# Kernel optimization log

Hardware: AMD Instinct MI355X
Metric: run time of the kernel (lower is better)

The kernel has to match this reference:

```python
import jax, jax.numpy as jnp
import numpy as np

EPS = 1e-5

def setup_inputs() -> dict:
    key = jax.random.key(0)
    k1, k2, k3 = jax.random.split(key, 3)
    B, T, D, K = 8, 4096, 256, 2048
    x = jax.random.normal(k1, (B, T, D), dtype=jnp.float32)
    embedding_sum = jax.random.normal(k2, (K, D), dtype=jnp.float32)
    cluster_usage = jax.random.uniform(k3, (K,), dtype=jnp.float32)
    return {"x": x, "embedding_sum": embedding_sum, "cluster_usage": cluster_usage}

def reference(x, embedding_sum, cluster_usage):
    # embedding = embedding_sum / clamp(cluster_usage, eps)  -> [K, D]
    emb = embedding_sum / jnp.clip(cluster_usage, EPS, None)[:, None]
    shape = x.shape
    flat = x.reshape(-1, shape[-1])  # [N, D]
    # squared Euclidean distances (argmin-equivalent to torch.cdist p=2)
    d = (
        jnp.sum(flat * flat, axis=-1, keepdims=True)
        - 2.0 * flat @ emb.T
        + jnp.sum(emb * emb, axis=-1)
    )  # [N, K]
    flat_codes = jnp.argmin(d, axis=-1)  # [N]
    codes = flat_codes.reshape(shape[:-1])  # [B, T]
    quantized = emb[codes]  # [B, T, D]
    return quantized, codes
```

## Files before the change

kernel.cpp:

```cpp
#include <hip/hip_runtime.h>


#define EPSV 1e-5f
#define TAU  0.4f
#define DDIM 256
#define BM   128
#define BCL  128
#define NPART 4
#define NCT  4
#define RPB  8
#define KSPL 4
#define NROWS 32768
#define EB   32

typedef __attribute__((ext_vector_type(8))) _Float16 f16x8;
typedef __attribute__((ext_vector_type(4))) float f32x4;
typedef unsigned short u16;
typedef unsigned u32;
typedef unsigned long long u64;

__device__ __forceinline__ u16 f2h(float f) {
    f = fminf(fmaxf(f, -60000.f), 60000.f);
    const _Float16 h = (_Float16)f;
    return __builtin_bit_cast(u16, h);
}
__device__ __forceinline__ u32 umn(u32 a, u32 b) { return a < b ? a : b; }
__device__ __forceinline__ u32 umx(u32 a, u32 b) { return a > b ? a : b; }
__device__ __forceinline__ float unsort(u32 u) {
    const u32 v = (u & 0x80000000u) ? (u & 0x7FFFFFFFu) : ~u;
    return __builtin_bit_cast(float, v);
}
__device__ __forceinline__ u64 packdk(float d, int k) {
    u32 u = __builtin_bit_cast(u32, d);
    u = (u & 0x80000000u) ? ~u : (u | 0x80000000u);
    return ((u64)u << 32) | (u32)k;
}

__global__ void prep(const float* __restrict__ esum,
                     const float* __restrict__ usage,
                     const float* __restrict__ x,
                     float* __restrict__ emb_t,
                     u16* __restrict__ eh,
                     float* __restrict__ enorm2,
                     u16* __restrict__ xh,
                     int* __restrict__ counter,
                     int K) {
    const int b = blockIdx.x;
    const int NEB = K / EB;
    if (b == 0 && threadIdx.x == 0) *counter = 0;
    if (b < NEB) {
        __shared__ float tile[EB][DDIM + 1];
        const int k0 = b * EB;
        const int d  = threadIdx.x;
        for (int r = 0; r < EB; ++r) {
            const int k = k0 + r;
            const float u = fmaxf(usage[k], EPSV);
            const float e = esum[(size_t)k * DDIM + d] / u;
            tile[r][d] = e;
            eh[(size_t)k * DDIM + d] = f2h(e);
        }
        __syncthreads();
        if (threadIdx.x < EB) {
            const int r = threadIdx.x;
            float s = 0.f;
            #pragma unroll 8
            for (int dd = 0; dd < DDIM; ++dd) {
                const float e = tile[r][dd];
                s = fmaf(e, e, s);
            }
            enorm2[k0 + r] = s;
        }
        for (int it = 0; it < DDIM / 8; ++it) {
            const int dd   = it * 8 + (threadIdx.x >> 5);
            const int lane = threadIdx.x & 31;
            emb_t[(size_t)dd * K + k0 + lane] = tile[lane][dd];
        }
    } else {
        const int n = (b - NEB) * 4 + (threadIdx.x >> 6);
        const int l = threadIdx.x & 63;
        const float4 v = *(const float4*)&x[(size_t)n * DDIM + l * 4];
        ushort4 h;
        h.x = f2h(v.x); h.y = f2h(v.y); h.z = f2h(v.z); h.w = f2h(v.w);
        *(ushort4*)&xh[(size_t)n * DDIM + l * 4] = h;
    }
}

__global__ __launch_bounds__(256, 2) void vq_mfma(
        const u16* __restrict__ xh, const u16* __restrict__ eh,
        const float* __restrict__ enorm2,
        u32* __restrict__ pp1, u32* __restrict__ pp2, int N) {
    __shared__ __align__(16) u16 Als[BM * 64];
    __shared__ __align__(16) u16 Bls[BCL * 64];

    const int tid = threadIdx.x;
    const int l   = tid & 63;
    const int w   = tid >> 6;
    const int wr  = w >> 1, wc = w & 1;

    const int nwg = (N / BM) * NPART;
    const int q   = nwg >> 3;
    const int pb  = blockIdx.x;
    const int logical = (pb & 7) * q + (pb >> 3);
    const int rowblk  = logical >> 2;
    const int part    = logical & 3;
    const int n0      = rowblk * BM;
    const int cbase   = part * 512;

    u32 m1p[4][4], m2p[4][4];
    #pragma unroll
    for (int a = 0; a < 4; ++a)
        #pragma unroll
        for (int b = 0; b < 4; ++b) { m1p[a][b] = 0xFFFFFFFFu; m2p[a][b] = 0xFFFFFFFFu; }

    const int sgc = (l & 7) ^ ((l >> 3) & 7);

    for (int ct = 0; ct < NCT; ++ct) {
        const int c0 = cbase + ct * BCL;
        f32x4 acc[4][4];
        #pragma unroll
        for (int a = 0; a < 4; ++a)
            #pragma unroll
            for (int b = 0; b < 4; ++b) acc[a][b] = (f32x4){0.f, 0.f, 0.f, 0.f};

        for (int ch = 0; ch < 4; ++ch) {
            const int colof = ch * 64;

            __syncthreads();
            #pragma unroll
            for (int j = 0; j < 4; ++j) {
                const int r = (w * 4 + j) * 8 + (l >> 3);
                const u16* ga = xh + (size_t)(n0 + r) * DDIM + colof + sgc * 8;
                __builtin_amdgcn_global_load_lds(
                    (const __attribute__((address_space(1))) void*)ga,
                    (__attribute__((address_space(3))) void*)((char*)Als + (w * 4 + j) * 1024),
                    16, 0, 0);
            }
            #pragma unroll
            for (int j = 0; j < 4; ++j) {
                const int r = (w * 4 + j) * 8 + (l >> 3);
                const u16* gb = eh + (size_t)(c0 + r) * DDIM + colof + sgc * 8;
                __builtin_amdgcn_global_load_lds(
                    (const __attribute__((address_space(1))) void*)gb,
                    (__attribute__((address_space(3))) void*)((char*)Bls + (w * 4 + j) * 1024),
                    16, 0, 0);
            }
            __syncthreads();

            #pragma unroll
            for (int ks = 0; ks < 2; ++ks) {
                f16x8 af[4], bfr[4];
                #pragma unroll
                for (int f = 0; f < 4; ++f) {
                    const int arow = wr * 64 + f * 16 + (l & 15);
                    const int ac   = (ks * 4 + (l >> 4)) ^ (l & 7);
                    af[f] = *(const f16x8*)((const char*)Als + arow * 128 + ac * 16);
                    const int brow = wc * 64 + f * 16 + (l & 15);
                    const int bc   = (ks * 4 + (l >> 4)) ^ (l & 7);
                    bfr[f] = *(const f16x8*)((const char*)Bls + brow * 128 + bc * 16);
                }
                #pragma unroll
                for (int fm = 0; fm < 4; ++fm)
                    #pragma unroll
                    for (int fn = 0; fn < 4; ++fn)
                        acc[fm][fn] = __builtin_amdgcn_mfma_f32_16x16x32_f16(
                            af[fm], bfr[fn], acc[fm][fn], 0, 0, 0);
            }
        }

        #pragma unroll
        for (int fn = 0; fn < 4; ++fn) {
            const int k = c0 + wc * 64 + fn * 16 + (l & 15);
            const float en = enorm2[k];
            #pragma unroll
            for (int fm = 0; fm < 4; ++fm)
                #pragma unroll
                for (int i = 0; i < 4; ++i) {
                    const float s = fmaf(-2.0f, acc[fm][fn][i], en);
                    u32 u = __builtin_bit_cast(u32, s);
                    u = ((int)u < 0) ? ~u : (u | 0x80000000u);
                    const u32 p = (u & 0xFFFFF800u) | (u32)k;
                    m2p[fm][i] = umn(m2p[fm][i], umx(p, m1p[fm][i]));
                    m1p[fm][i] = umn(m1p[fm][i], p);
                }
        }
    }

    #pragma unroll
    for (int fm = 0; fm < 4; ++fm)
        #pragma unroll
        for (int i = 0; i < 4; ++i) {
            u32 p1 = m1p[fm][i], p2 = m2p[fm][i];
            #pragma unroll
            for (int mask = 1; mask < 16; mask <<= 1) {
                const u32 o1 = (u32)__shfl_xor((int)p1, mask, 64);
                const u32 o2 = (u32)__shfl_xor((int)p2, mask, 64);
                p2 = umn(umn(p2, o2), umx(p1, o1));
                p1 = umn(p1, o1);
            }
            m1p[fm][i] = p1; m2p[fm][i] = p2;
        }

    __syncthreads();
    u32* S1 = (u32*)Als;
    u32* S2 = (u32*)((char*)Als + 512);
    if (wc == 0 && (l & 15) == 0) {
        #pragma unroll
        for (int fm = 0; fm < 4; ++fm)
            #pragma unroll
            for (int i = 0; i < 4; ++i) {
                const int r = wr * 64 + fm * 16 + (l >> 4) * 4 + i;
                S1[r] = m1p[fm][i]; S2[r] = m2p[fm][i];
            }
    }
    __syncthreads();
    if (wc == 1 && (l & 15) == 0) {
        #pragma unroll
        for (int fm = 0; fm < 4; ++fm)
            #pragma unroll
            for (int i = 0; i < 4; ++i) {
                const int r = wr * 64 + fm * 16 + (l >> 4) * 4 + i;
                const u32 o1 = S1[r], o2 = S2[r];
                u32 p1 = m1p[fm][i], p2 = m2p[fm][i];
                const u32 M2 = umn(umn(p2, o2), umx(p1, o1));
                const u32 M1 = umn(p1, o1);
                const int n = n0 + r;
                pp1[(size_t)part * N + n] = M1;
                pp2[(size_t)part * N + n] = M2;
            }
    }
}

__global__ void combine(const u32* __restrict__ pp1, const u32* __restrict__ pp2,
                        int* __restrict__ codes_i, int* __restrict__ flags,
                        int* __restrict__ list, int* __restrict__ counter,
                        u64* __restrict__ packed, int N) {
    const int n = blockIdx.x * 256 + threadIdx.x;
    u32 p1 = pp1[n], p2 = pp2[n];
    #pragma unroll
    for (int j = 1; j < NPART; ++j) {
        const u32 o1 = pp1[(size_t)j * N + n], o2 = pp2[(size_t)j * N + n];
        p2 = umn(umn(p2, o2), umx(p1, o1));
        p1 = umn(p1, o1);
    }
    codes_i[n] = (int)(p1 & 0x7FFu);
    const float m1f = unsort(p1 & 0xFFFFF800u);
    const float m2f = unsort(p2 & 0xFFFFF800u);
    const int fl = (m2f - m1f < TAU) ? 1 : 0;
    flags[n] = fl;
    if (fl) {
        packed[n] = 0xFFFFFFFFFFFFFFFFull;
        const int idx = atomicAdd(counter, 1);
        list[idx] = n;
    }
}

__global__ __launch_bounds__(256) void rescue_c(
        const float* __restrict__ x, const float* __restrict__ emb_t,
        const float* __restrict__ enorm2,
        const int* __restrict__ list, const int* __restrict__ counter,
        u64* __restrict__ packed, int K) {
    __shared__ float xs[RPB][DDIM];
    const int t = threadIdx.x;
    const int l = t & 63;
    int cnt = *counter;
    cnt = cnt < 0 ? 0 : (cnt > NROWS ? NROWS : cnt);
    if (cnt == 0) return;
    const int nblk  = (cnt + RPB - 1) / RPB;
    const int items = nblk * KSPL;
    const int kc    = K / KSPL;

    for (int wi = blockIdx.x; wi < items; wi += gridDim.x) {
        const int g = wi >> 2;
        const int q = wi & 3;
        const int base = g * RPB;
        int rows[RPB];
        #pragma unroll
        for (int r = 0; r < RPB; ++r) {
            int idx = base + r;
            rows[r] = list[idx < cnt ? idx : cnt - 1];
        }
        __syncthreads();
        #pragma unroll
        for (int r = 0; r < RPB; ++r)
            xs[r][t] = x[(size_t)rows[r] * DDIM + t];
        __syncthreads();

        float acc[RPB][2];
        #pragma unroll
        for (int r = 0; r < RPB; ++r) { acc[r][0] = 0.f; acc[r][1] = 0.f; }

        const float* eb = emb_t + q * kc + 2 * t;
        #pragma unroll 4
        for (int d = 0; d < DDIM; ++d) {
            const float2 e = *(const float2*)&eb[(size_t)d * K];
            #pragma unroll
            for (int r = 0; r < RPB; ++r) {
                const float xv = xs[r][d];
                acc[r][0] = fmaf(xv, e.x, acc[r][0]);
                acc[r][1] = fmaf(xv, e.y, acc[r][1]);
            }
        }

        const int k0 = q * kc + 2 * t;
        const float en0 = enorm2[k0], en1 = enorm2[k0 + 1];
        #pragma unroll
        for (int r = 0; r < RPB; ++r) {
            const float s0 = fmaf(-2.0f, acc[r][0], en0);
            const float s1 = fmaf(-2.0f, acc[r][1], en1);
            float bd = s0; int bk = k0;
            if (s1 < bd) { bd = s1; bk = k0 + 1; }
            #pragma unroll
            for (int m = 1; m < 64; m <<= 1) {
                const float od = __shfl_xor(bd, m, 64);
                const int   ok = __shfl_xor(bk, m, 64);
                if (od < bd || (od == bd && ok < bk)) { bd = od; bk = ok; }
            }
            if (l == 0) atomicMin(&packed[rows[r]], packdk(bd, bk));
        }
    }
}

__global__ void gather_q(const float* __restrict__ esum,
                         const float* __restrict__ usage,
                         const int* __restrict__ codes_i,
                         const int* __restrict__ flags,
                         const u64* __restrict__ packed,
                         float* __restrict__ qout,
                         float* __restrict__ codes_f) {
    const int n = blockIdx.x * 4 + (threadIdx.x >> 6);
    const int c = threadIdx.x & 63;
    int k = codes_i[n];
    if (flags[n]) k = (int)(packed[n] & 0xFFFFFFFFull);
    if (c == 0) codes_f[n] = (float)k;
    const float u = fmaxf(usage[k], EPSV);
    float4 v = *(const float4*)&esum[(size_t)k * DDIM + c * 4];
    v.x /= u; v.y /= u; v.z /= u; v.w /= u;
    *(float4*)&qout[(size_t)n * DDIM + c * 4] = v;
}

extern "C" void kernel_launch(void* const* d_in, const int* in_sizes, int n_in,
                              void* d_out, int out_size, void* d_ws, size_t ws_size,
                              hipStream_t stream) {
    const float* x     = (const float*)d_in[0];
    const float* esum  = (const float*)d_in[1];
    const float* usage = (const float*)d_in[2];
    const int K = in_sizes[2];
    const int N = in_sizes[0] / DDIM;

    char* p = (char*)d_ws;
    u64*   packed  = (u64*)p;                  p += (size_t)N * 8;
    float* emb_t   = (float*)p;                p += (size_t)K * DDIM * 4;
    float* enorm2  = (float*)p;                p += (size_t)K * 4;
    u32*   pp1     = (u32*)p;                  p += (size_t)NPART * N * 4;
    u32*   pp2     = (u32*)p;                  p += (size_t)NPART * N * 4;
    int*   codes_i = (int*)p;                  p += (size_t)N * 4;
    int*   flags   = (int*)p;                  p += (size_t)N * 4;
    int*   list    = (int*)p;                  p += (size_t)N * 4;
    int*   counter = (int*)p;                  p += 256;
    u16*   xh      = (u16*)p;                  p += (size_t)N * DDIM * 2;
    u16*   eh      = (u16*)p;                  p += (size_t)K * DDIM * 2;

    float* qout    = (float*)d_out;
    float* codes_f = qout + (size_t)N * DDIM;

    prep<<<K / EB + N / 4, 256, 0, stream>>>(esum, usage, x, emb_t, eh,
                                             enorm2, xh, counter, K);
    vq_mfma<<<(N / BM) * NPART, 256, 0, stream>>>(xh, eh, enorm2, pp1, pp2, N);
    combine<<<N / 256, 256, 0, stream>>>(pp1, pp2, codes_i, flags,
                                         list, counter, packed, N);
    rescue_c<<<1024, 256, 0, stream>>>(x, emb_t, enorm2, list, counter, packed, K);
    gather_q<<<N / 4, 256, 0, stream>>>(esum, usage, codes_i, flags, packed,
                                        qout, codes_f);
}
```

Before: 117.3 us.

## Double-buffer MFMA LDS tiles and restructure rescue kernel to read x directly

The MFMA distance kernel now keeps two LDS buffers for the A and B tiles and prefetches the next k-chunk with global_load_lds while the current one is computed, replacing the two full syncthreads per chunk with partial vmcnt waits and barriers. The rescue kernel doubles rows per block, drops its shared-memory staging of x, and reads x values straight from global memory (wave-uniform broadcast loads), unrolling d by two. The goal is to overlap global-to-LDS transfers with MFMA work and to cut LDS traffic and syncs in the rescue path. The cost is twice the LDS footprint, which may lower occupancy, plus more global loads and higher register pressure in the rescue loop.

```diff
diff --git a/kernel.cpp b/kernel.cpp
--- a/kernel.cpp
+++ b/kernel.cpp
@@ -8,7 +8,7 @@
 #define BCL  128
 #define NPART 4
 #define NCT  4
-#define RPB  8
+#define RPB  16
 #define KSPL 4
 #define NROWS 32768
 #define EB   32
@@ -89,8 +89,8 @@
         const u16* __restrict__ xh, const u16* __restrict__ eh,
         const float* __restrict__ enorm2,
         u32* __restrict__ pp1, u32* __restrict__ pp2, int N) {
-    __shared__ __align__(16) u16 Als[BM * 64];
-    __shared__ __align__(16) u16 Bls[BCL * 64];
+    __shared__ __align__(16) u16 Als[2][BM * 64];
+    __shared__ __align__(16) u16 Bls[2][BCL * 64];
 
     const int tid = threadIdx.x;
     const int l   = tid & 63;
@@ -114,6 +114,28 @@
 
     const int sgc = (l & 7) ^ ((l >> 3) & 7);
 
+    auto stage = [&](int rr) {
+        const int buf   = rr & 1;
+        const int c0    = cbase + (rr >> 2) * BCL;
+        const int colof = (rr & 3) * 64;
+        #pragma unroll
+        for (int j = 0; j < 4; ++j) {
+            const int r = (w * 4 + j) * 8 + (l >> 3);
+            const u16* ga = xh + (size_t)(n0 + r) * DDIM + colof + sgc * 8;
+            __builtin_amdgcn_global_load_lds(
+                (const __attribute__((address_space(1))) void*)ga,
+                (__attribute__((address_space(3))) void*)((char*)Als[buf] + (w * 4 + j) * 1024),
+                16, 0, 0);
+            const u16* gb = eh + (size_t)(c0 + r) * DDIM + colof + sgc * 8;
+            __builtin_amdgcn_global_load_lds(
+                (const __attribute__((address_space(1))) void*)gb,
+                (__attribute__((address_space(3))) void*)((char*)Bls[buf] + (w * 4 + j) * 1024),
+                16, 0, 0);
+        }
+    };
+
+    stage(0);
+    int rr = 0;
     for (int ct = 0; ct < NCT; ++ct) {
         const int c0 = cbase + ct * BCL;
         f32x4 acc[4][4];
@@ -122,29 +144,14 @@
             #pragma unroll
             for (int b = 0; b < 4; ++b) acc[a][b] = (f32x4){0.f, 0.f, 0.f, 0.f};
 
-        for (int ch = 0; ch < 4; ++ch) {
-            const int colof = ch * 64;
-
-            __syncthreads();
-            #pragma unroll
-            for (int j = 0; j < 4; ++j) {
-                const int r = (w * 4 + j) * 8 + (l >> 3);
-                const u16* ga = xh + (size_t)(n0 + r) * DDIM + colof + sgc * 8;
-                __builtin_amdgcn_global_load_lds(
-                    (const __attribute__((address_space(1))) void*)ga,
-                    (__attribute__((address_space(3))) void*)((char*)Als + (w * 4 + j) * 1024),
-                    16, 0, 0);
-            }
-            #pragma unroll
-            for (int j = 0; j < 4; ++j) {
-                const int r = (w * 4 + j) * 8 + (l >> 3);
-                const u16* gb = eh + (size_t)(c0 + r) * DDIM + colof + sgc * 8;
-                __builtin_amdgcn_global_load_lds(
-                    (const __attribute__((address_space(1))) void*)gb,
-                    (__attribute__((address_space(3))) void*)((char*)Bls + (w * 4 + j) * 1024),
-                    16, 0, 0);
-            }
-            __syncthreads();
+        for (int ch = 0; ch < 4; ++ch, ++rr) {
+            if (rr + 1 < NCT * 4) {
+                stage(rr + 1);
+                asm volatile("s_waitcnt vmcnt(8)\n\ts_barrier" ::: "memory");
+            } else {
+                asm volatile("s_waitcnt vmcnt(0)\n\ts_barrier" ::: "memory");
+            }
+            const int buf = rr & 1;
 
             #pragma unroll
             for (int ks = 0; ks < 2; ++ks) {
@@ -153,10 +160,10 @@
                 for (int f = 0; f < 4; ++f) {
                     const int arow = wr * 64 + f * 16 + (l & 15);
                     const int ac   = (ks * 4 + (l >> 4)) ^ (l & 7);
-                    af[f] = *(const f16x8*)((const char*)Als + arow * 128 + ac * 16);
+                    af[f] = *(const f16x8*)((const char*)Als[buf] + arow * 128 + ac * 16);
                     const int brow = wc * 64 + f * 16 + (l & 15);
                     const int bc   = (ks * 4 + (l >> 4)) ^ (l & 7);
-                    bfr[f] = *(const f16x8*)((const char*)Bls + brow * 128 + bc * 16);
+                    bfr[f] = *(const f16x8*)((const char*)Bls[buf] + brow * 128 + bc * 16);
                 }
                 #pragma unroll
                 for (int fm = 0; fm < 4; ++fm)
@@ -165,6 +172,7 @@
                         acc[fm][fn] = __builtin_amdgcn_mfma_f32_16x16x32_f16(
                             af[fm], bfr[fn], acc[fm][fn], 0, 0, 0);
             }
+            asm volatile("s_waitcnt lgkmcnt(0)\n\ts_barrier" ::: "memory");
         }
 
         #pragma unroll
@@ -259,7 +267,6 @@
         const float* __restrict__ enorm2,
         const int* __restrict__ list, const int* __restrict__ counter,
         u64* __restrict__ packed, int K) {
-    __shared__ float xs[RPB][DDIM];
     const int t = threadIdx.x;
     const int l = t & 63;
     int cnt = *counter;
@@ -277,27 +284,26 @@
         #pragma unroll
         for (int r = 0; r < RPB; ++r) {
             int idx = base + r;
-            rows[r] = list[idx < cnt ? idx : cnt - 1];
-        }
-        __syncthreads();
-        #pragma unroll
-        for (int r = 0; r < RPB; ++r)
-            xs[r][t] = x[(size_t)rows[r] * DDIM + t];
-        __syncthreads();
+            if (idx >= cnt) idx = cnt - 1;
+            rows[r] = list[idx];
+        }
 
         float acc[RPB][2];
         #pragma unroll
         for (int r = 0; r < RPB; ++r) { acc[r][0] = 0.f; acc[r][1] = 0.f; }
 
         const float* eb = emb_t + q * kc + 2 * t;
-        #pragma unroll 4
-        for (int d = 0; d < DDIM; ++d) {
-            const float2 e = *(const float2*)&eb[(size_t)d * K];
+        for (int d = 0; d < DDIM; d += 2) {
+            const float2 e0 = *(const float2*)&eb[(size_t)d * K];
+            const float2 e1 = *(const float2*)&eb[(size_t)(d + 1) * K];
             #pragma unroll
             for (int r = 0; r < RPB; ++r) {
-                const float xv = xs[r][d];
-                acc[r][0] = fmaf(xv, e.x, acc[r][0]);
-                acc[r][1] = fmaf(xv, e.y, acc[r][1]);
+                const float xv0 = x[(size_t)rows[r] * DDIM + d];
+                const float xv1 = x[(size_t)rows[r] * DDIM + d + 1];
+                acc[r][0] = fmaf(xv0, e0.x, acc[r][0]);
+                acc[r][1] = fmaf(xv0, e0.y, acc[r][1]);
+                acc[r][0] = fmaf(xv1, e1.x, acc[r][0]);
+                acc[r][1] = fmaf(xv1, e1.y, acc[r][1]);
             }
         }
 
```

Measured after the change: 151.7 us. 29.4% more time.
